# Kernel tuning notes

Hardware: AMD Instinct MI355X
Metric: run time of the kernel (lower is better)

## Reference

```python
import jax, jax.numpy as jnp
import numpy as np

N_REF, N_IN, D_FEAT, P, N_ELEM = 4096, 8192, 512, 256, 4


def setup_inputs() -> dict:
    key = jax.random.key(0)
    k1, k2, k3, k4, k5 = jax.random.split(key, 5)
    return {
        "Alpha": jax.random.normal(k1, (P, N_REF), dtype=jnp.float32) * 0.05,
        "X_ref": jax.random.normal(k2, (N_REF, D_FEAT), dtype=jnp.float32),
        "desc": jax.random.normal(k3, (N_IN, D_FEAT), dtype=jnp.float32),
        "Z_ref": jax.random.randint(k4, (N_REF,), 0, N_ELEM, dtype=jnp.int32),
        "Z": jax.random.randint(k5, (N_IN,), 0, N_ELEM, dtype=jnp.int32),
        "expK": 2,
    }


def reference(Alpha, X_ref, desc, Z_ref, Z, expK):
    # Per-element grouped kernel: K[i, j] = (X_ref[i] . desc[j])**expK,
    # contribution only where ref atom i and query atom j share the element.
    # This is exactly the gather -> per-element GEMM+pow -> combine -> scatter
    # of the original module, expressed as one masked dense computation.
    K = jnp.power(jnp.matmul(X_ref, desc.T), expK)          # [N_ref, N_in]
    same_elem = Z_ref[:, None] == Z[None, :]                # [N_ref, N_in]
    K_masked = jnp.where(same_elem, K, jnp.zeros((), K.dtype))
    y = jnp.matmul(Alpha, K_masked)                          # [P, N_in]
    return y
```

## Files before the change

kernel.cpp:

```cpp
#include <hip/hip_runtime.h>
#include <stdint.h>

#define P_DIM 256
#define NREF  4096
#define NIN   8192
#define DF    512
#define NE    4
#define CREF  1536
#define CIN   2560
#define AE_LD (NE * CREF)
#define ROWB  416
#define ALPB  96

typedef __bf16 bf16x8 __attribute__((ext_vector_type(8)));
typedef float  f32x4  __attribute__((ext_vector_type(4)));
typedef unsigned short ush8 __attribute__((ext_vector_type(8)));

static __device__ __forceinline__ unsigned short f2bf(float f) {
    uint32_t u = __builtin_bit_cast(uint32_t, f);
    u += 0x7FFFu + ((u >> 16) & 1u);
    return (unsigned short)(u >> 16);
}

__global__ __launch_bounds__(256) void prep(
    const float* __restrict__ Alpha, const float* __restrict__ X_ref,
    const float* __restrict__ desc,
    const int* __restrict__ Zr, const int* __restrict__ Z,
    unsigned short* __restrict__ Xe, unsigned short* __restrict__ De,
    unsigned short* __restrict__ Ae,
    int* __restrict__ jperm_ws, int* __restrict__ cnt_ws) {
    __shared__ unsigned short ipermL[NE * CREF];
    __shared__ unsigned short jpermL[NE * CIN];
    __shared__ int hist[2 * NE * 256];
    __shared__ int cntS[2 * NE];
    const int t = threadIdx.x;
    constexpr int CHX = NREF / 256, CHD = NIN / 256;

    int lc[NE];
#pragma unroll
    for (int e = 0; e < NE; ++e) lc[e] = 0;
    for (int k = 0; k < CHX; ++k) lc[Zr[t * CHX + k] & (NE - 1)]++;
#pragma unroll
    for (int e = 0; e < NE; ++e) hist[e * 256 + t] = lc[e];
#pragma unroll
    for (int e = 0; e < NE; ++e) lc[e] = 0;
    for (int k = 0; k < CHD; ++k) lc[Z[t * CHD + k] & (NE - 1)]++;
#pragma unroll
    for (int e = 0; e < NE; ++e) hist[(NE + e) * 256 + t] = lc[e];
    __syncthreads();
    if (t < 2 * NE) {
        int run = 0;
        for (int u = 0; u < 256; ++u) {
            int v = hist[t * 256 + u]; hist[t * 256 + u] = run; run += v;
        }
        cntS[t] = (t < NE) ? (run > CREF ? CREF : run) : (run > CIN ? CIN : run);
    }
    __syncthreads();
    int off[NE];
#pragma unroll
    for (int e = 0; e < NE; ++e) off[e] = hist[e * 256 + t];
    for (int k = 0; k < CHX; ++k) {
        int i = t * CHX + k;
        int e = Zr[i] & (NE - 1);
        int o = off[e]++;
        if (o < CREF) ipermL[e * CREF + o] = (unsigned short)i;
    }
#pragma unroll
    for (int e = 0; e < NE; ++e) off[e] = hist[(NE + e) * 256 + t];
    for (int k = 0; k < CHD; ++k) {
        int j = t * CHD + k;
        int e = Z[j] & (NE - 1);
        int o = off[e]++;
        if (o < CIN) jpermL[e * CIN + o] = (unsigned short)j;
    }
    __syncthreads();

    if (blockIdx.x == 0) {
        for (int idx = t; idx < NE * CIN; idx += 256)
            jperm_ws[idx] = jpermL[idx];
        if (t < 2 * NE) cnt_ws[t] = cntS[t];
    }

    if (blockIdx.x < ROWB) {
        int gw = (blockIdx.x * 256 + t) >> 6;
        int lane = t & 63;
        constexpr int NW = ROWB * 4;
        for (int w = gw; w < NE * (CREF + CIN); w += NW) {
            const float* src = nullptr;
            unsigned short* dst;
            if (w < NE * CREF) {
                int e = w / CREF, s = w - e * CREF;
                if (s < cntS[e]) src = X_ref + (size_t)ipermL[w] * DF;
                dst = Xe + (size_t)w * DF;
            } else {
                int w2 = w - NE * CREF;
                int e = w2 / CIN, s = w2 - e * CIN;
                if (s < cntS[NE + e]) src = desc + (size_t)jpermL[w2] * DF;
                dst = De + (size_t)w2 * DF;
            }
            ush8 o;
            if (src) {
                float4 a = *(const float4*)(src + lane * 8);
                float4 b = *(const float4*)(src + lane * 8 + 4);
                o[0] = f2bf(a.x); o[1] = f2bf(a.y); o[2] = f2bf(a.z); o[3] = f2bf(a.w);
                o[4] = f2bf(b.x); o[5] = f2bf(b.y); o[6] = f2bf(b.z); o[7] = f2bf(b.w);
            } else {
                o = (ush8){0, 0, 0, 0, 0, 0, 0, 0};
            }
            *(ush8*)(dst + lane * 8) = o;
        }
    } else {
        int b2 = blockIdx.x - ROWB;
        int colb = b2 % (AE_LD / 256);
        int pr = b2 / (AE_LD / 256);
        int col = colb * 256 + t;
        int e = col / CREF, ic = col - e * CREF;
        int src = (ic < cntS[e]) ? (int)ipermL[col] : -1;
        const int pend = pr * 64 + 64;
        for (int p = pr * 64; p < pend; ++p) {
            unsigned short v = 0;
            if (src >= 0) v = f2bf(Alpha[(size_t)p * NREF + src]);
            Ae[(size_t)p * AE_LD + col] = v;
        }
    }
}

__global__ __launch_bounds__(256) void g1_grouped(
    const unsigned short* __restrict__ DeA, const unsigned short* __restrict__ XeA,
    unsigned short* __restrict__ KtA, const int* __restrict__ cnt) {
    constexpr int BK = 64;
    const int e = blockIdx.z;
    const int padR = (cnt[e] + 127) & ~127;
    const int padI = (cnt[NE + e] + 127) & ~127;
    const int m0 = blockIdx.y * 128;
    const int n0 = blockIdx.x * 128;
    if (m0 >= padI || n0 >= padR) return;

    const unsigned short* A = DeA + (size_t)e * CIN * DF;
    const unsigned short* B = XeA + (size_t)e * CREF * DF;
    unsigned short* C = KtA + (size_t)e * CIN * CREF;

    __shared__ unsigned short tA[128 * BK];
    __shared__ unsigned short tB[128 * BK];

    const int tid = threadIdx.x, wave = tid >> 6, lane = tid & 63;
    const int waveM = (wave >> 1) * 64, waveN = (wave & 1) * 64;
    const int lrow = lane >> 3, ls = lane & 7;
    const int l15 = lane & 15, lq = lane >> 4;

    f32x4 acc[4][4];
#pragma unroll
    for (int r = 0; r < 4; ++r)
#pragma unroll
        for (int c = 0; c < 4; ++c) acc[r][c] = (f32x4){0.f, 0.f, 0.f, 0.f};

#pragma unroll 1
    for (int k0 = 0; k0 < DF; k0 += BK) {
        __syncthreads();
#pragma unroll
        for (int it = 0; it < 8; ++it) {
            int cb = wave + it * 4;
            bool isB = cb >= 16;
            int cb2 = isB ? cb - 16 : cb;
            int row = cb2 * 8 + lrow;
            int g = ls ^ (row & 7);
            const unsigned short* gp = (isB ? B : A)
                + (size_t)((isB ? n0 : m0) + row) * DF + (size_t)(k0 + g * 8);
            unsigned short* lp = (isB ? tB : tA) + cb2 * (8 * BK);
            __builtin_amdgcn_global_load_lds(
                (const __attribute__((address_space(1))) void*)gp,
                (__attribute__((address_space(3))) void*)lp, 16, 0, 0);
        }
        __syncthreads();
#pragma unroll
        for (int kk = 0; kk < BK; kk += 32) {
            const int cbase = kk >> 3;
            bf16x8 af[4], bf[4];
#pragma unroll
            for (int r = 0; r < 4; ++r) {
                int m = waveM + r * 16 + l15;
                int ch = (cbase + lq) ^ (m & 7);
                af[r] = *(const bf16x8*)&tA[m * BK + ch * 8];
            }
#pragma unroll
            for (int c = 0; c < 4; ++c) {
                int n = waveN + c * 16 + l15;
                int ch = (cbase + lq) ^ (n & 7);
                bf[c] = *(const bf16x8*)&tB[n * BK + ch * 8];
            }
#pragma unroll
            for (int r = 0; r < 4; ++r)
#pragma unroll
                for (int c = 0; c < 4; ++c)
                    acc[r][c] = __builtin_amdgcn_mfma_f32_16x16x32_bf16(
                        af[r], bf[c], acc[r][c], 0, 0, 0);
        }
    }

#pragma unroll
    for (int r = 0; r < 4; ++r) {
        int mb = m0 + waveM + r * 16 + lq * 4;
#pragma unroll
        for (int reg = 0; reg < 4; ++reg) {
            size_t ro = (size_t)(mb + reg) * CREF;
#pragma unroll
            for (int c = 0; c < 4; ++c) {
                int n = n0 + waveN + c * 16 + l15;
                float v = acc[r][c][reg];
                C[ro + n] = f2bf(v * v);
            }
        }
    }
}

__global__ __launch_bounds__(256) void g2_grouped(
    const unsigned short* __restrict__ Ae, const unsigned short* __restrict__ KtA,
    const int* __restrict__ jperm, const int* __restrict__ cnt,
    float* __restrict__ out) {
    constexpr int BK = 64;
    const int e = blockIdx.z;
    const int cntI = cnt[NE + e];
    const int padR = (cnt[e] + 127) & ~127;
    const int n0 = blockIdx.x * 64;
    const int m0 = blockIdx.y * 128;
    if (n0 >= cntI) return;

    const unsigned short* B = KtA + (size_t)e * CIN * CREF;
    __shared__ unsigned short tA[128 * BK];
    __shared__ unsigned short tB[64 * BK];

    const int tid = threadIdx.x, wave = tid >> 6, lane = tid & 63;
    const int waveM = (wave >> 1) * 64, waveN = (wave & 1) * 32;
    const int lrow = lane >> 3, ls = lane & 7;
    const int l15 = lane & 15, lq = lane >> 4;

    f32x4 acc[4][2];
#pragma unroll
    for (int r = 0; r < 4; ++r)
#pragma unroll
        for (int c = 0; c < 2; ++c) acc[r][c] = (f32x4){0.f, 0.f, 0.f, 0.f};

#pragma unroll 1
    for (int k0 = 0; k0 < padR; k0 += BK) {
        __syncthreads();
#pragma unroll
        for (int it = 0; it < 6; ++it) {
            int cb = wave + it * 4;
            bool isB = cb >= 16;
            int cb2 = isB ? cb - 16 : cb;
            int row = cb2 * 8 + lrow;
            int g = ls ^ (row & 7);
            const unsigned short* gp = isB
                ? B + (size_t)(n0 + row) * CREF + (size_t)(k0 + g * 8)
                : Ae + (size_t)(m0 + row) * AE_LD + (size_t)(e * CREF + k0 + g * 8);
            unsigned short* lp = (isB ? tB : tA) + cb2 * (8 * BK);
            __builtin_amdgcn_global_load_lds(
                (const __attribute__((address_space(1))) void*)gp,
                (__attribute__((address_space(3))) void*)lp, 16, 0, 0);
        }
        __syncthreads();
#pragma unroll
        for (int kk = 0; kk < BK; kk += 32) {
            const int cbase = kk >> 3;
            bf16x8 af[4], bf[2];
#pragma unroll
            for (int r = 0; r < 4; ++r) {
                int m = waveM + r * 16 + l15;
                int ch = (cbase + lq) ^ (m & 7);
                af[r] = *(const bf16x8*)&tA[m * BK + ch * 8];
            }
#pragma unroll
            for (int c = 0; c < 2; ++c) {
                int n = waveN + c * 16 + l15;
                int ch = (cbase + lq) ^ (n & 7);
                bf[c] = *(const bf16x8*)&tB[n * BK + ch * 8];
            }
#pragma unroll
            for (int r = 0; r < 4; ++r)
#pragma unroll
                for (int c = 0; c < 2; ++c)
                    acc[r][c] = __builtin_amdgcn_mfma_f32_16x16x32_bf16(
                        af[r], bf[c], acc[r][c], 0, 0, 0);
        }
    }

    int jok[2], jdest[2];
#pragma unroll
    for (int c = 0; c < 2; ++c) {
        int jl = n0 + waveN + c * 16 + l15;
        jok[c] = jl < cntI;
        jdest[c] = jok[c] ? jperm[e * CIN + jl] : 0;
    }
#pragma unroll
    for (int r = 0; r < 4; ++r) {
        int pb = m0 + waveM + r * 16 + lq * 4;
#pragma unroll
        for (int reg = 0; reg < 4; ++reg) {
            size_t ro = (size_t)(pb + reg) * NIN;
#pragma unroll
            for (int c = 0; c < 2; ++c)
                if (jok[c]) out[ro + jdest[c]] = acc[r][c][reg];
        }
    }
}

extern "C" void kernel_launch(void* const* d_in, const int* in_sizes, int n_in,
                              void* d_out, int out_size, void* d_ws, size_t ws_size,
                              hipStream_t stream) {
    const float* Alpha = (const float*)d_in[0];
    const float* X_ref = (const float*)d_in[1];
    const float* desc  = (const float*)d_in[2];
    const int*   Z_ref = (const int*)d_in[3];
    const int*   Z     = (const int*)d_in[4];
    float* out = (float*)d_out;

    unsigned short* Xe = (unsigned short*)d_ws;
    unsigned short* De = Xe + (size_t)NE * CREF * DF;
    unsigned short* Ae = De + (size_t)NE * CIN * DF;
    unsigned short* Kt = Ae + (size_t)P_DIM * AE_LD;
    int* jperm = (int*)(Kt + (size_t)NE * CIN * CREF);
    int* cnt   = jperm + NE * CIN;

    prep<<<ROWB + ALPB, 256, 0, stream>>>(Alpha, X_ref, desc, Z_ref, Z,
                                          Xe, De, Ae, jperm, cnt);

    g1_grouped<<<dim3(CREF / 128, CIN / 128, NE), 256, 0, stream>>>(
        De, Xe, Kt, cnt);

    g2_grouped<<<dim3(CIN / 64, P_DIM / 128, NE), 256, 0, stream>>>(
        Ae, Kt, jperm, cnt, out);
}
```

Before: 167.9 us.

## Split prep into single-block sort plus wide gather/convert kernel

```diff
diff --git a/kernel.cpp b/kernel.cpp
--- a/kernel.cpp
+++ b/kernel.cpp
@@ -9,8 +9,7 @@
 #define CREF  1536
 #define CIN   2560
 #define AE_LD (NE * CREF)
-#define ROWB  416
-#define ALPB  96
+#define GROWB 4096
 
 typedef __bf16 bf16x8 __attribute__((ext_vector_type(8)));
 typedef float  f32x4  __attribute__((ext_vector_type(4)));
@@ -22,18 +21,12 @@
     return (unsigned short)(u >> 16);
 }
 
-__global__ __launch_bounds__(256) void prep(
-    const float* __restrict__ Alpha, const float* __restrict__ X_ref,
-    const float* __restrict__ desc,
+__global__ __launch_bounds__(256) void plan_sort(
     const int* __restrict__ Zr, const int* __restrict__ Z,
-    unsigned short* __restrict__ Xe, unsigned short* __restrict__ De,
-    unsigned short* __restrict__ Ae,
-    int* __restrict__ jperm_ws, int* __restrict__ cnt_ws) {
-    __shared__ unsigned short ipermL[NE * CREF];
-    __shared__ unsigned short jpermL[NE * CIN];
+    int* __restrict__ iperm, int* __restrict__ jperm, int* __restrict__ cnt) {
     __shared__ int hist[2 * NE * 256];
     __shared__ int cntS[2 * NE];
-    const int t = threadIdx.x;
+    const int t = threadIdx.x, wv = t >> 6, ln = t & 63;
     constexpr int CHX = NREF / 256, CHD = NIN / 256;
 
     int lc[NE];
@@ -48,14 +41,26 @@
 #pragma unroll
     for (int e = 0; e < NE; ++e) hist[(NE + e) * 256 + t] = lc[e];
     __syncthreads();
-    if (t < 2 * NE) {
-        int run = 0;
-        for (int u = 0; u < 256; ++u) {
-            int v = hist[t * 256 + u]; hist[t * 256 + u] = run; run += v;
-        }
-        cntS[t] = (t < NE) ? (run > CREF ? CREF : run) : (run > CIN ? CIN : run);
+
+    for (int row = wv; row < 2 * NE; row += 4) {
+        int* h = hist + row * 256;
+        int v0 = h[ln * 4], v1 = h[ln * 4 + 1], v2 = h[ln * 4 + 2], v3 = h[ln * 4 + 3];
+        int s = v0 + v1 + v2 + v3, sc = s;
+#pragma unroll
+        for (int d = 1; d < 64; d <<= 1) {
+            int u = __shfl_up(sc, d, 64);
+            if (ln >= d) sc += u;
+        }
+        int ex = sc - s;
+        h[ln * 4] = ex;
+        h[ln * 4 + 1] = ex + v0;
+        h[ln * 4 + 2] = ex + v0 + v1;
+        h[ln * 4 + 3] = ex + v0 + v1 + v2;
+        if (ln == 63)
+            cntS[row] = (row < NE) ? (sc > CREF ? CREF : sc) : (sc > CIN ? CIN : sc);
     }
     __syncthreads();
+
     int off[NE];
 #pragma unroll
     for (int e = 0; e < NE; ++e) off[e] = hist[e * 256 + t];
@@ -63,7 +68,7 @@
         int i = t * CHX + k;
         int e = Zr[i] & (NE - 1);
         int o = off[e]++;
-        if (o < CREF) ipermL[e * CREF + o] = (unsigned short)i;
+        if (o < CREF) iperm[e * CREF + o] = i;
     }
 #pragma unroll
     for (int e = 0; e < NE; ++e) off[e] = hist[(NE + e) * 256 + t];
@@ -71,57 +76,53 @@
         int j = t * CHD + k;
         int e = Z[j] & (NE - 1);
         int o = off[e]++;
-        if (o < CIN) jpermL[e * CIN + o] = (unsigned short)j;
-    }
-    __syncthreads();
-
-    if (blockIdx.x == 0) {
-        for (int idx = t; idx < NE * CIN; idx += 256)
-            jperm_ws[idx] = jpermL[idx];
-        if (t < 2 * NE) cnt_ws[t] = cntS[t];
-    }
-
-    if (blockIdx.x < ROWB) {
-        int gw = (blockIdx.x * 256 + t) >> 6;
+        if (o < CIN) jperm[e * CIN + o] = j;
+    }
+    if (t < 2 * NE) cnt[t] = cntS[t];
+}
+
+__global__ __launch_bounds__(256) void gather_alpha(
+    const float* __restrict__ Alpha, const float* __restrict__ X_ref,
+    const float* __restrict__ desc,
+    const int* __restrict__ iperm, const int* __restrict__ jperm,
+    const int* __restrict__ cnt,
+    unsigned short* __restrict__ Xe, unsigned short* __restrict__ De,
+    unsigned short* __restrict__ Ae) {
+    const int t = threadIdx.x;
+    if (blockIdx.x < GROWB) {
+        int w = blockIdx.x * 4 + (t >> 6);
         int lane = t & 63;
-        constexpr int NW = ROWB * 4;
-        for (int w = gw; w < NE * (CREF + CIN); w += NW) {
-            const float* src = nullptr;
-            unsigned short* dst;
-            if (w < NE * CREF) {
-                int e = w / CREF, s = w - e * CREF;
-                if (s < cntS[e]) src = X_ref + (size_t)ipermL[w] * DF;
-                dst = Xe + (size_t)w * DF;
-            } else {
-                int w2 = w - NE * CREF;
-                int e = w2 / CIN, s = w2 - e * CIN;
-                if (s < cntS[NE + e]) src = desc + (size_t)jpermL[w2] * DF;
-                dst = De + (size_t)w2 * DF;
-            }
-            ush8 o;
-            if (src) {
-                float4 a = *(const float4*)(src + lane * 8);
-                float4 b = *(const float4*)(src + lane * 8 + 4);
-                o[0] = f2bf(a.x); o[1] = f2bf(a.y); o[2] = f2bf(a.z); o[3] = f2bf(a.w);
-                o[4] = f2bf(b.x); o[5] = f2bf(b.y); o[6] = f2bf(b.z); o[7] = f2bf(b.w);
-            } else {
-                o = (ush8){0, 0, 0, 0, 0, 0, 0, 0};
-            }
-            *(ush8*)(dst + lane * 8) = o;
-        }
+        const float* src = nullptr;
+        unsigned short* dst;
+        if (w < NE * CREF) {
+            int e = w / CREF, s = w - e * CREF;
+            if (s < cnt[e]) src = X_ref + (size_t)iperm[w] * DF;
+            dst = Xe + (size_t)w * DF;
+        } else {
+            int w2 = w - NE * CREF;
+            int e = w2 / CIN, s = w2 - e * CIN;
+            if (s < cnt[NE + e]) src = desc + (size_t)jperm[w2] * DF;
+            dst = De + (size_t)w2 * DF;
+        }
+        ush8 o;
+        if (src) {
+            float4 a = *(const float4*)(src + lane * 8);
+            float4 b = *(const float4*)(src + lane * 8 + 4);
+            o[0] = f2bf(a.x); o[1] = f2bf(a.y); o[2] = f2bf(a.z); o[3] = f2bf(a.w);
+            o[4] = f2bf(b.x); o[5] = f2bf(b.y); o[6] = f2bf(b.z); o[7] = f2bf(b.w);
+        } else {
+            o = (ush8){0, 0, 0, 0, 0, 0, 0, 0};
+        }
+        *(ush8*)(dst + lane * 8) = o;
     } else {
-        int b2 = blockIdx.x - ROWB;
-        int colb = b2 % (AE_LD / 256);
-        int pr = b2 / (AE_LD / 256);
-        int col = colb * 256 + t;
-        int e = col / CREF, ic = col - e * CREF;
-        int src = (ic < cntS[e]) ? (int)ipermL[col] : -1;
-        const int pend = pr * 64 + 64;
-        for (int p = pr * 64; p < pend; ++p) {
-            unsigned short v = 0;
-            if (src >= 0) v = f2bf(Alpha[(size_t)p * NREF + src]);
-            Ae[(size_t)p * AE_LD + col] = v;
-        }
+        int idx = (blockIdx.x - GROWB) * 256 + t;
+        int p = idx / AE_LD;
+        int col = idx - p * AE_LD;
+        int e = col / CREF;
+        int ic = col - e * CREF;
+        unsigned short v = 0;
+        if (ic < cnt[e]) v = f2bf(Alpha[(size_t)p * NREF + iperm[col]]);
+        Ae[idx] = v;
     }
 }
 
@@ -318,11 +319,14 @@
     unsigned short* De = Xe + (size_t)NE * CREF * DF;
     unsigned short* Ae = De + (size_t)NE * CIN * DF;
     unsigned short* Kt = Ae + (size_t)P_DIM * AE_LD;
-    int* jperm = (int*)(Kt + (size_t)NE * CIN * CREF);
+    int* iperm = (int*)(Kt + (size_t)NE * CIN * CREF);
+    int* jperm = iperm + NE * CREF;
     int* cnt   = jperm + NE * CIN;
 
-    prep<<<ROWB + ALPB, 256, 0, stream>>>(Alpha, X_ref, desc, Z_ref, Z,
-                                          Xe, De, Ae, jperm, cnt);
+    plan_sort<<<1, 256, 0, stream>>>(Z_ref, Z, iperm, jperm, cnt);
+
+    gather_alpha<<<GROWB + P_DIM * AE_LD / 256, 256, 0, stream>>>(
+        Alpha, X_ref, desc, iperm, jperm, cnt, Xe, De, Ae);
 
     g1_grouped<<<dim3(CREF / 128, CIN / 128, NE), 256, 0, stream>>>(
         De, Xe, Kt, cnt);
```

New measurement: 153.7 us. 1.09x faster.
